# Performance work log

Hardware: AMD Instinct MI355X
Metric: run time of the kernel (lower is better)

## Reference

```python
import jax, jax.numpy as jnp
import numpy as np
import math
from functools import lru_cache

LMAX = 2
MUL = 64
BATCH = 1024
# all parity-allowed paths for lmax=2, in the module's enumeration order
PATHS = [(0,0,0),(0,1,1),(0,2,2),(1,0,1),(1,1,0),(1,1,2),(1,2,1),(2,0,2),(2,1,1),(2,2,0),(2,2,2)]

# ---- CG tensor construction (numpy, float64), faithful port of the torch source ----

def _counts(L):
    return [(a, b, L - a - b) for a in range(L, -1, -1) for b in range(L - a, -1, -1)]

def _dfact(n):
    out = 1
    for k in range(n, 0, -2):
        out *= k
    return out

def _gmom(n):
    return 0.0 if n % 2 == 1 else float(_dfact(n - 1))

@lru_cache(maxsize=None)
def _gram(L):
    c = _counts(L)
    D = len(c)
    G = np.zeros((D, D))
    for i, (a, b, cc) in enumerate(c):
        for j, (a2, b2, c2) in enumerate(c):
            G[i, j] = _gmom(a + a2) * _gmom(b + b2) * _gmom(cc + c2)
    return G

@lru_cache(maxsize=None)
def _laplacian(L):
    cL = _counts(L)
    cS = _counts(L - 2)
    idxS = {t: i for i, t in enumerate(cS)}
    M = np.zeros((len(cS), len(cL)))
    for j, (a, b, c) in enumerate(cL):
        if a >= 2: M[idxS[(a - 2, b, c)], j] += a * (a - 1)
        if b >= 2: M[idxS[(a, b - 2, c)], j] += b * (b - 1)
        if c >= 2: M[idxS[(a, b, c - 2)], j] += c * (c - 1)
    return M

@lru_cache(maxsize=None)
def _harm_basis(L):
    # harmonic basis in monomial coords: null space of Laplacian, whitened by Gaussian Gram
    if L == 0:
        return np.ones((1, 1))
    if L == 1:
        return np.eye(3)
    Delta = _laplacian(L)
    _, s, vh = np.linalg.svd(Delta, full_matrices=True)
    rank = int((s > 1e-12).sum())
    B = vh[rank:].T
    G = _gram(L)
    M = B.T @ G @ B
    ev, evec = np.linalg.eigh(M)
    ev = np.clip(ev, 1e-14, None)
    W = evec @ np.diag(ev ** -0.5) @ evec.T
    return B @ W

@lru_cache(maxsize=None)
def _r2k_lift(l, k):
    # multiply Sym^l polynomial by (x^2+y^2+z^2)^k -> Sym^{l+2k}
    cl = _counts(l)
    cL = _counts(l + 2 * k)
    idxL = {t: i for i, t in enumerate(cL)}
    M = np.zeros((len(cL), len(cl)))
    for i in range(k + 1):
        for j in range(k - i + 1):
            h = k - i - j
            coef = math.factorial(k) / (math.factorial(i) * math.factorial(j) * math.factorial(h))
            for col, (a, b, c) in enumerate(cl):
                M[idxL[(a + 2 * i, b + 2 * j, c + 2 * h)], col] += coef
    return M

@lru_cache(maxsize=None)
def _poly_mult(l1, l2, L):
    c1, c2, cL = _counts(l1), _counts(l2), _counts(L)
    idxL = {t: i for i, t in enumerate(cL)}
    M = np.zeros((len(cL), len(c1) * len(c2)))
    for i, a in enumerate(c1):
        for j, b in enumerate(c2):
            M[idxL[(a[0] + b[0], a[1] + b[1], a[2] + b[2])], i * len(c2) + j] = 1.0
    return M

@lru_cache(maxsize=None)
def _projector(L, l):
    # P_{L->l}: monomial coeffs of Sym^L -> harmonic coords of Harm^l
    k = (L - l) // 2
    GL = _gram(L)
    Bl = _harm_basis(l)
    V = _r2k_lift(l, k) @ Bl
    G = V.T @ GL @ V
    return np.linalg.solve(G, V.T @ GL)

@lru_cache(maxsize=None)
def _cg(l1, l2, l3):
    L = l1 + l2
    P = _projector(L, l3)
    B1, B2 = _harm_basis(l1), _harm_basis(l2)
    Mp = _poly_mult(l1, l2, L)
    m1, m2 = 2 * l1 + 1, 2 * l2 + 1
    outer = np.einsum('im,jn->ijmn', B1, B2).reshape(B1.shape[0] * B2.shape[0], m1 * m2)
    C = (P @ (Mp @ outer)).T.reshape(m1, m2, 2 * l3 + 1)
    n = np.linalg.norm(C)
    if n > 1e-30:  # 'component' normalization
        C = C * (math.sqrt(2 * l3 + 1) / n)
    return C


def setup_inputs() -> dict:
    key = jax.random.key(0)
    ks = jax.random.split(key, 7)
    inp = {}
    for l in range(LMAX + 1):
        inp[f'x1_l{l}'] = jax.random.normal(ks[l], (BATCH, MUL, 2 * l + 1), dtype=jnp.float32)
        inp[f'x2_l{l}'] = jax.random.normal(ks[l + 3], (BATCH, MUL, 2 * l + 1), dtype=jnp.float32)
    inp['W'] = jax.random.normal(ks[6], (len(PATHS), MUL, MUL, MUL), dtype=jnp.float32) * 0.02
    for p, (l1, l2, l3) in enumerate(PATHS):
        inp[f'C_{p}'] = jnp.asarray(_cg(l1, l2, l3), dtype=jnp.float32)
    return inp


def reference(x1_l0, x1_l1, x1_l2, x2_l0, x2_l1, x2_l2, W,
              C_0, C_1, C_2, C_3, C_4, C_5, C_6, C_7, C_8, C_9, C_10):
    x1 = {0: x1_l0, 1: x1_l1, 2: x1_l2}
    x2 = {0: x2_l0, 1: x2_l1, 2: x2_l2}
    Cs = [C_0, C_1, C_2, C_3, C_4, C_5, C_6, C_7, C_8, C_9, C_10]
    B = x1_l0.shape[0]
    mul_out = W.shape[1]
    out = {l: jnp.zeros((B, mul_out, 2 * l + 1), dtype=x1_l0.dtype) for l in range(LMAX + 1)}
    for p, (l1, l2, l3) in enumerate(PATHS):
        # out[z,w,k] += sum_{u,v,m,n} x1[z,u,m] x2[z,v,n] W[p,w,u,v] C[p][m,n,k]
        out[l3] = out[l3] + jnp.einsum('zum,zvn,wuv,mnk->zwk',
                                       x1[l1], x2[l2], W[p], Cs[p], optimize='optimal')
    # concatenate the output irrep dict l -> (B, mul_out, 2l+1) along the m axis
    return jnp.concatenate([out[l] for l in range(LMAX + 1)], axis=-1)
```

## Files before the change

kernel.cpp:

```cpp
#include <hip/hip_runtime.h>
#include <hip/hip_bf16.h>


#define NTHREADS 256
#define SMEM_BYTES 32768

typedef __attribute__((ext_vector_type(4))) float f32x4;
typedef __attribute__((ext_vector_type(8))) short s16x8;

__device__ __forceinline__ unsigned short f2bf(float x) {
    union { float f; unsigned u; } v; v.f = x;
    unsigned r = v.u + 0x7fffu + ((v.u >> 16) & 1u);
    return (unsigned short)(r >> 16);
}
__device__ __forceinline__ unsigned pk2bf(float a, float b) {
    union { __hip_bfloat162 h; unsigned u; } v;
    v.h = __float22bfloat162_rn(make_float2(a, b));
    return v.u;
}


__global__ __launch_bounds__(NTHREADS) void prep_w(const float* __restrict__ W,
                                                   unsigned short* __restrict__ Wb)
{
    int id = blockIdx.x * NTHREADS + threadIdx.x;
    int v4 = (id & 15) << 2;
    int w  = (id >> 4) & 63;
    int u  = (id >> 10) & 63;
    int p  = id >> 16;
    float4 f = *(const float4*)(W + (((size_t)p * 64 + w) * 64 + u) * 64 + v4);
    ushort4 h;
    h.x = f2bf(f.x); h.y = f2bf(f.y); h.z = f2bf(f.z); h.w = f2bf(f.w);
    *(ushort4*)(Wb + (((size_t)p * 64 + u) * 64 + w) * 64 + v4) = h;
}


struct KArgs {
    const float*          x1[3];
    const float*          x2[3];
    const unsigned short* Wb;
    const float*          C[11];
    float*                part[11];
};

template <int M1, int N1, int K1, int ZT, int S1, int UC>
__device__ __forceinline__ void run_path(const float* __restrict__ x1g,
                                         const float* __restrict__ x2g,
                                         const unsigned short* __restrict__ Wbp,
                                         const float* __restrict__ Cg,
                                         float* __restrict__ partp,
                                         int local, char* __restrict__ smem)
{
    constexpr int KN   = K1 * N1;
    constexpr int NC   = ZT * K1 / 16;
    constexpr bool EVEN = (NC % 2 == 0);
    constexpr int ROWT = EVEN ? 2 : 1;
    constexpr int COLT = EVEN ? NC / 2 : NC;
    constexpr int PASSES = ZT / 8;
    constexpr int SST  = UC * S1 + 4;
    constexpr int TROWS = ZT * K1;
    static_assert(512 + ZT * SST * 4 + 2 * TROWS * 72 * 2 <= SMEM_BYTES, "LDS");

    float*          sC  = (float*)smem;
    float*          sc1 = (float*)(smem + 512);
    unsigned short* sT0 = (unsigned short*)(smem + 512 + ZT * SST * 4);

    const int t = threadIdx.x, lane = t & 63, wave = t >> 6;
    const int ln = lane & 15, q = lane >> 4;
    const int zz = lane >> 5, vp = lane & 31;
    const int ztile = local >> 2, usub = local & 3;
    const int z0 = ztile * ZT, u0 = usub * 16;

    for (int i = t; i < M1 * N1 * K1; i += NTHREADS) sC[i] = Cg[i];
    __syncthreads();

    auto build_slab = [&](int us0) {
        for (int i = t; i < ZT * UC * KN; i += NTHREADS) {
            int z   = i / (UC * KN);
            int r   = i - z * (UC * KN);
            int uu2 = r / KN;
            int j   = r - uu2 * KN;
            int k   = j / N1, n = j - k * N1;
            const float* x1r = x1g + ((size_t)(z0 + z) * 64 + u0 + us0 + uu2) * M1;
            float s = 0.f;
#pragma unroll
            for (int m = 0; m < M1; ++m) s += x1r[m] * sC[(m * N1 + n) * K1 + k];
            sc1[z * SST + uu2 * S1 + j] = s;
        }
    };

    float xr[PASSES][2][N1];
#pragma unroll
    for (int p = 0; p < PASSES; ++p) {
        const int z = z0 + p * 8 + wave * 2 + zz;
        const float* xp = x2g + ((size_t)z * 64 + 2 * vp) * N1;
#pragma unroll
        for (int j = 0; j < 2 * N1; ++j) xr[p][j / N1][j % N1] = xp[j];
    }

    auto tform = [&](int uf, unsigned short* sTn) {
        const int uus = uf % UC;
#pragma unroll
        for (int p = 0; p < PASSES; ++p) {
            const int z = p * 8 + wave * 2 + zz;
            const float4* cp = (const float4*)&sc1[z * SST + uus * S1];
            float c1v[S1];
#pragma unroll
            for (int jj = 0; jj < S1 / 4; ++jj) {
                float4 f = cp[jj];
                c1v[jj * 4 + 0] = f.x; c1v[jj * 4 + 1] = f.y;
                c1v[jj * 4 + 2] = f.z; c1v[jj * 4 + 3] = f.w;
            }
#pragma unroll
            for (int k = 0; k < K1; ++k) {
                float s0 = 0.f, s1 = 0.f;
#pragma unroll
                for (int n = 0; n < N1; ++n) {
                    const float cv = c1v[k * N1 + n];
                    s0 += xr[p][0][n] * cv;
                    s1 += xr[p][1][n] * cv;
                }
                *(unsigned*)&sTn[(z * K1 + k) * 72 + 2 * vp] = pk2bf(s0, s1);
            }
        }
    };

    f32x4 acc[ROWT][COLT];
#pragma unroll
    for (int rt = 0; rt < ROWT; ++rt)
#pragma unroll
        for (int ci = 0; ci < COLT; ++ci) acc[rt][ci] = (f32x4){0.f, 0.f, 0.f, 0.f};

    build_slab(0);
    __syncthreads();
    tform(0, sT0);
    __syncthreads();

#pragma unroll 2
    for (int uu = 0; uu < 16; ++uu) {
        if (((uu + 1) % UC) == 0 && (uu + 1) < 16) {
            build_slab(uu + 1);
            __syncthreads();
        }
        const int cur = uu & 1;
        unsigned short* sTc = sT0 + cur * (TROWS * 72);
        unsigned short* sTn = sT0 + (cur ^ 1) * (TROWS * 72);

        const unsigned short* wsrc = Wbp + (size_t)(u0 + uu) * 4096;
        s16x8 areg[ROWT][2];
#pragma unroll
        for (int rt = 0; rt < ROWT; ++rt) {
            const int wt = EVEN ? ((wave >> 1) * 2 + rt) : wave;
#pragma unroll
            for (int s2 = 0; s2 < 2; ++s2)
                areg[rt][s2] = *(const s16x8*)(wsrc + (wt * 16 + ln) * 64 + s2 * 32 + q * 8);
        }

        if (uu < 15) tform(uu + 1, sTn);

#pragma unroll
        for (int ci = 0; ci < COLT; ++ci) {
            const int c = EVEN ? ((wave & 1) * COLT + ci) : ci;
            s16x8 bf0 = *(const s16x8*)&sTc[(c * 16 + ln) * 72 + q * 8];
            s16x8 bf1 = *(const s16x8*)&sTc[(c * 16 + ln) * 72 + 32 + q * 8];
#pragma unroll
            for (int rt = 0; rt < ROWT; ++rt) {
                acc[rt][ci] = __builtin_amdgcn_mfma_f32_16x16x32_bf16(
                    areg[rt][0], bf0, acc[rt][ci], 0, 0, 0);
                acc[rt][ci] = __builtin_amdgcn_mfma_f32_16x16x32_bf16(
                    areg[rt][1], bf1, acc[rt][ci], 0, 0, 0);
            }
        }
        __syncthreads();
    }

#pragma unroll
    for (int rt = 0; rt < ROWT; ++rt) {
        const int wt = EVEN ? ((wave >> 1) * 2 + rt) : wave;
#pragma unroll
        for (int ci = 0; ci < COLT; ++ci) {
            const int c = EVEN ? ((wave & 1) * COLT + ci) : ci;
            const int col = c * 16 + ln;
            const int z = col / K1, k = col - z * K1;
            float* op = partp + ((size_t)(usub * 1024 + z0 + z) * 64) * K1 + k;
#pragma unroll
            for (int r = 0; r < 4; ++r)
                op[(wt * 16 + q * 4 + r) * K1] = acc[rt][ci][r];
        }
    }
}

__global__ __launch_bounds__(NTHREADS, 5) void tp_main(KArgs a)
{
    __shared__ __align__(16) char smem[SMEM_BYTES];

    const int bid = blockIdx.x;
    const int starts[12] = {0, 256, 512, 768, 1024, 1280, 1408, 1536, 1664, 1792, 1920, 2048};
    int idx = 0;
#pragma unroll
    for (int i = 1; i < 12; ++i) idx += (bid >= starts[i]) ? 1 : 0;
    const int local = bid - starts[idx];

    switch (idx) {
        case 0:  run_path<1,5,5,16,28, 4>(a.x1[0], a.x2[2], a.Wb + (size_t) 2*262144, a.C[2],  a.part[2],  local, smem); break;
        case 1:  run_path<5,5,5,16,28, 4>(a.x1[2], a.x2[2], a.Wb + (size_t)10*262144, a.C[10], a.part[10], local, smem); break;
        case 2:  run_path<3,3,5,16,16, 8>(a.x1[1], a.x2[1], a.Wb + (size_t) 5*262144, a.C[5],  a.part[5],  local, smem); break;
        case 3:  run_path<5,1,5,16, 8,16>(a.x1[2], a.x2[0], a.Wb + (size_t) 7*262144, a.C[7],  a.part[7],  local, smem); break;
        case 4:  run_path<3,5,3,16,16, 8>(a.x1[1], a.x2[2], a.Wb + (size_t) 6*262144, a.C[6],  a.part[6],  local, smem); break;
        case 5:  run_path<1,3,3,32,12, 2>(a.x1[0], a.x2[1], a.Wb + (size_t) 1*262144, a.C[1],  a.part[1],  local, smem); break;
        case 6:  run_path<5,3,3,32,12, 2>(a.x1[2], a.x2[1], a.Wb + (size_t) 8*262144, a.C[8],  a.part[8],  local, smem); break;
        case 7:  run_path<3,1,3,32, 4, 8>(a.x1[1], a.x2[0], a.Wb + (size_t) 3*262144, a.C[3],  a.part[3],  local, smem); break;
        case 8:  run_path<5,5,1,32, 8,16>(a.x1[2], a.x2[2], a.Wb + (size_t) 9*262144, a.C[9],  a.part[9],  local, smem); break;
        case 9:  run_path<3,3,1,32, 4,16>(a.x1[1], a.x2[1], a.Wb + (size_t) 4*262144, a.C[4],  a.part[4],  local, smem); break;
        case 10: run_path<1,1,1,32, 4,16>(a.x1[0], a.x2[0], a.Wb + (size_t) 0*262144, a.C[0],  a.part[0],  local, smem); break;
        default: break;
    }
}


struct RArgs {
    const float* part[11];
    float*       out;
};

__global__ __launch_bounds__(NTHREADS) void reduce_out(RArgs r)
{
    const int g   = blockIdx.x >> 8;
    const int tid = (blockIdx.x & 255) * NTHREADS + threadIdx.x;
    float* op = r.out + (size_t)tid * 9;

    if (g == 0) {
        const int P[3] = {0, 4, 9};
        float o = 0.f;
#pragma unroll
        for (int pi = 0; pi < 3; ++pi) {
            const float* pp = r.part[P[pi]];
#pragma unroll
            for (int us = 0; us < 4; ++us)
                o += pp[(size_t)(us * 65536) + tid];
        }
        op[0] = o;
    } else if (g == 1) {
        const int P[4] = {1, 3, 6, 8};
        float o[3] = {0.f, 0.f, 0.f};
#pragma unroll
        for (int pi = 0; pi < 4; ++pi) {
            const float* pp = r.part[P[pi]];
#pragma unroll
            for (int us = 0; us < 4; ++us) {
                const float* row = pp + ((size_t)(us * 65536) + tid) * 3;
#pragma unroll
                for (int k = 0; k < 3; ++k) o[k] += row[k];
            }
        }
#pragma unroll
        for (int k = 0; k < 3; ++k) op[1 + k] = o[k];
    } else {
        const int P[4] = {2, 5, 7, 10};
        float o[5] = {0.f, 0.f, 0.f, 0.f, 0.f};
#pragma unroll
        for (int pi = 0; pi < 4; ++pi) {
            const float* pp = r.part[P[pi]];
#pragma unroll
            for (int us = 0; us < 4; ++us) {
                const float* row = pp + ((size_t)(us * 65536) + tid) * 5;
#pragma unroll
                for (int k = 0; k < 5; ++k) o[k] += row[k];
            }
        }
#pragma unroll
        for (int k = 0; k < 5; ++k) op[4 + k] = o[k];
    }
}


extern "C" void kernel_launch(void* const* d_in, const int* in_sizes, int n_in,
                              void* d_out, int out_size, void* d_ws, size_t ws_size,
                              hipStream_t stream)
{
    static const int cumK1[11] = {0, 1, 4, 9, 12, 13, 18, 21, 26, 29, 30};

    unsigned short* Wb = (unsigned short*)d_ws;
    float* partbase = (float*)((char*)d_ws + (6u << 20));

    KArgs a;
    a.x1[0] = (const float*)d_in[0];
    a.x2[0] = (const float*)d_in[1];
    a.x1[1] = (const float*)d_in[2];
    a.x2[1] = (const float*)d_in[3];
    a.x1[2] = (const float*)d_in[4];
    a.x2[2] = (const float*)d_in[5];
    a.Wb = Wb;
    RArgs rr;
    for (int p = 0; p < 11; ++p) {
        a.C[p]    = (const float*)d_in[7 + p];
        a.part[p] = partbase + (size_t)cumK1[p] * 262144;
        rr.part[p] = a.part[p];
    }
    rr.out = (float*)d_out;

    prep_w<<<dim3(720896 / NTHREADS), NTHREADS, 0, stream>>>((const float*)d_in[6], Wb);
    tp_main<<<dim3(2048), NTHREADS, 0, stream>>>(a);
    reduce_out<<<dim3(768), NTHREADS, 0, stream>>>(rr);
}
```

Baseline: 183.7 us.

## Process two u-steps per pipeline iteration to halve barriers, retune path tiles

The main loop now packs two u-slices into each double-buffered LDS tile (row stride 136 instead of 72). This halves the number of iterations and __syncthreads barriers, and each B row feeds four MFMAs per iteration. Several path configurations drop ZT from 32 to 16 and change UC, so the grid grows to 2432 blocks. The cost is a larger LDS footprint (about 50KB) with launch bounds lowered from 5 to 3 blocks per SM, which reduces occupancy.

Result: no change. 184.6 us (+0.5%).

```diff
diff --git a/kernel.cpp b/kernel.cpp
--- a/kernel.cpp
+++ b/kernel.cpp
@@ -3,7 +3,7 @@
 
 
 #define NTHREADS 256
-#define SMEM_BYTES 32768
+#define SMEM_BYTES 51456
 
 typedef __attribute__((ext_vector_type(4))) float f32x4;
 typedef __attribute__((ext_vector_type(8))) short s16x8;
@@ -59,7 +59,7 @@
     constexpr int PASSES = ZT / 8;
     constexpr int SST  = UC * S1 + 4;
     constexpr int TROWS = ZT * K1;
-    static_assert(512 + ZT * SST * 4 + 2 * TROWS * 72 * 2 <= SMEM_BYTES, "LDS");
+    static_assert(512 + ZT * SST * 4 + 2 * TROWS * 136 * 2 <= SMEM_BYTES, "LDS");
 
     float*          sC  = (float*)smem;
     float*          sc1 = (float*)(smem + 512);
@@ -100,6 +100,7 @@
 
     auto tform = [&](int uf, unsigned short* sTn) {
         const int uus = uf % UC;
+        const int coff = (uf & 1) * 64 + 2 * vp;
 #pragma unroll
         for (int p = 0; p < PASSES; ++p) {
             const int z = p * 8 + wave * 2 + zz;
@@ -120,7 +121,7 @@
                     s0 += xr[p][0][n] * cv;
                     s1 += xr[p][1][n] * cv;
                 }
-                *(unsigned*)&sTn[(z * K1 + k) * 72 + 2 * vp] = pk2bf(s0, s1);
+                *(unsigned*)&sTn[(z * K1 + k) * 136 + coff] = pk2bf(s0, s1);
             }
         }
     };
@@ -134,41 +135,46 @@
     build_slab(0);
     __syncthreads();
     tform(0, sT0);
+    tform(1, sT0);
     __syncthreads();
 
-#pragma unroll 2
-    for (int uu = 0; uu < 16; ++uu) {
-        if (((uu + 1) % UC) == 0 && (uu + 1) < 16) {
-            build_slab(uu + 1);
+#pragma unroll 1
+    for (int it = 0; it < 8; ++it) {
+        if (((2 * it + 2) % UC) == 0 && it < 7) {
+            build_slab(2 * it + 2);
             __syncthreads();
         }
-        const int cur = uu & 1;
-        unsigned short* sTc = sT0 + cur * (TROWS * 72);
-        unsigned short* sTn = sT0 + (cur ^ 1) * (TROWS * 72);
-
-        const unsigned short* wsrc = Wbp + (size_t)(u0 + uu) * 4096;
-        s16x8 areg[ROWT][2];
-#pragma unroll
-        for (int rt = 0; rt < ROWT; ++rt) {
-            const int wt = EVEN ? ((wave >> 1) * 2 + rt) : wave;
-#pragma unroll
-            for (int s2 = 0; s2 < 2; ++s2)
-                areg[rt][s2] = *(const s16x8*)(wsrc + (wt * 16 + ln) * 64 + s2 * 32 + q * 8);
-        }
-
-        if (uu < 15) tform(uu + 1, sTn);
+        const int cur = it & 1;
+        unsigned short* sTc = sT0 + cur * (TROWS * 136);
+        unsigned short* sTn = sT0 + (cur ^ 1) * (TROWS * 136);
+
+        s16x8 areg[ROWT][4];
+#pragma unroll
+        for (int us = 0; us < 2; ++us) {
+            const unsigned short* wsrc = Wbp + (size_t)(u0 + 2 * it + us) * 4096;
+#pragma unroll
+            for (int rt = 0; rt < ROWT; ++rt) {
+                const int wt = EVEN ? ((wave >> 1) * 2 + rt) : wave;
+#pragma unroll
+                for (int s2 = 0; s2 < 2; ++s2)
+                    areg[rt][us * 2 + s2] =
+                        *(const s16x8*)(wsrc + (wt * 16 + ln) * 64 + s2 * 32 + q * 8);
+            }
+        }
+
+        if (it < 7) { tform(2 * it + 2, sTn); tform(2 * it + 3, sTn); }
 
 #pragma unroll
         for (int ci = 0; ci < COLT; ++ci) {
             const int c = EVEN ? ((wave & 1) * COLT + ci) : ci;
-            s16x8 bf0 = *(const s16x8*)&sTc[(c * 16 + ln) * 72 + q * 8];
-            s16x8 bf1 = *(const s16x8*)&sTc[(c * 16 + ln) * 72 + 32 + q * 8];
-#pragma unroll
-            for (int rt = 0; rt < ROWT; ++rt) {
-                acc[rt][ci] = __builtin_amdgcn_mfma_f32_16x16x32_bf16(
-                    areg[rt][0], bf0, acc[rt][ci], 0, 0, 0);
-                acc[rt][ci] = __builtin_amdgcn_mfma_f32_16x16x32_bf16(
-                    areg[rt][1], bf1, acc[rt][ci], 0, 0, 0);
+            const unsigned short* brow = &sTc[(c * 16 + ln) * 136];
+#pragma unroll
+            for (int c4 = 0; c4 < 4; ++c4) {
+                s16x8 bf = *(const s16x8*)(brow + c4 * 32 + q * 8);
+#pragma unroll
+                for (int rt = 0; rt < ROWT; ++rt)
+                    acc[rt][ci] = __builtin_amdgcn_mfma_f32_16x16x32_bf16(
+                        areg[rt][c4], bf, acc[rt][ci], 0, 0, 0);
             }
         }
         __syncthreads();
@@ -190,12 +196,12 @@
     }
 }
 
-__global__ __launch_bounds__(NTHREADS, 5) void tp_main(KArgs a)
+__global__ __launch_bounds__(NTHREADS, 3) void tp_main(KArgs a)
 {
     __shared__ __align__(16) char smem[SMEM_BYTES];
 
     const int bid = blockIdx.x;
-    const int starts[12] = {0, 256, 512, 768, 1024, 1280, 1408, 1536, 1664, 1792, 1920, 2048};
+    const int starts[12] = {0, 256, 512, 768, 1024, 1280, 1536, 1792, 2048, 2176, 2304, 2432};
     int idx = 0;
 #pragma unroll
     for (int i = 1; i < 12; ++i) idx += (bid >= starts[i]) ? 1 : 0;
@@ -204,12 +210,12 @@
     switch (idx) {
         case 0:  run_path<1,5,5,16,28, 4>(a.x1[0], a.x2[2], a.Wb + (size_t) 2*262144, a.C[2],  a.part[2],  local, smem); break;
         case 1:  run_path<5,5,5,16,28, 4>(a.x1[2], a.x2[2], a.Wb + (size_t)10*262144, a.C[10], a.part[10], local, smem); break;
-        case 2:  run_path<3,3,5,16,16, 8>(a.x1[1], a.x2[1], a.Wb + (size_t) 5*262144, a.C[5],  a.part[5],  local, smem); break;
-        case 3:  run_path<5,1,5,16, 8,16>(a.x1[2], a.x2[0], a.Wb + (size_t) 7*262144, a.C[7],  a.part[7],  local, smem); break;
+        case 2:  run_path<3,3,5,16,16, 4>(a.x1[1], a.x2[1], a.Wb + (size_t) 5*262144, a.C[5],  a.part[5],  local, smem); break;
+        case 3:  run_path<5,1,5,16, 8, 8>(a.x1[2], a.x2[0], a.Wb + (size_t) 7*262144, a.C[7],  a.part[7],  local, smem); break;
         case 4:  run_path<3,5,3,16,16, 8>(a.x1[1], a.x2[2], a.Wb + (size_t) 6*262144, a.C[6],  a.part[6],  local, smem); break;
-        case 5:  run_path<1,3,3,32,12, 2>(a.x1[0], a.x2[1], a.Wb + (size_t) 1*262144, a.C[1],  a.part[1],  local, smem); break;
-        case 6:  run_path<5,3,3,32,12, 2>(a.x1[2], a.x2[1], a.Wb + (size_t) 8*262144, a.C[8],  a.part[8],  local, smem); break;
-        case 7:  run_path<3,1,3,32, 4, 8>(a.x1[1], a.x2[0], a.Wb + (size_t) 3*262144, a.C[3],  a.part[3],  local, smem); break;
+        case 5:  run_path<1,3,3,16,12, 8>(a.x1[0], a.x2[1], a.Wb + (size_t) 1*262144, a.C[1],  a.part[1],  local, smem); break;
+        case 6:  run_path<5,3,3,16,12, 8>(a.x1[2], a.x2[1], a.Wb + (size_t) 8*262144, a.C[8],  a.part[8],  local, smem); break;
+        case 7:  run_path<3,1,3,16, 4,16>(a.x1[1], a.x2[0], a.Wb + (size_t) 3*262144, a.C[3],  a.part[3],  local, smem); break;
         case 8:  run_path<5,5,1,32, 8,16>(a.x1[2], a.x2[2], a.Wb + (size_t) 9*262144, a.C[9],  a.part[9],  local, smem); break;
         case 9:  run_path<3,3,1,32, 4,16>(a.x1[1], a.x2[1], a.Wb + (size_t) 4*262144, a.C[4],  a.part[4],  local, smem); break;
         case 10: run_path<1,1,1,32, 4,16>(a.x1[0], a.x2[0], a.Wb + (size_t) 0*262144, a.C[0],  a.part[0],  local, smem); break;
@@ -300,6 +306,6 @@
     rr.out = (float*)d_out;
 
     prep_w<<<dim3(720896 / NTHREADS), NTHREADS, 0, stream>>>((const float*)d_in[6], Wb);
-    tp_main<<<dim3(2048), NTHREADS, 0, stream>>>(a);
+    tp_main<<<dim3(2432), NTHREADS, 0, stream>>>(a);
     reduce_out<<<dim3(768), NTHREADS, 0, stream>>>(rr);
 }
```
